# Kernel optimization log

Measured on AMD Instinct MI355X. Metric: run time of the kernel, lower is better.

The kernel has to match this reference:

```python
import jax, jax.numpy as jnp
import numpy as np

N_NODES = 65536
IN_DIM = 256
HIDDEN = 256
NUM_GRAPHS = 128   # B = batch.max()+1; fixed by construction in setup_inputs
MAX_LEN = 1024     # >= max per-graph length (avg 512, binomial tail << 1024)


def _uniform(key, shape, scale):
    return jax.random.uniform(key, shape, jnp.float32, -scale, scale)


def setup_inputs() -> dict:
    key = jax.random.key(0)
    ks = jax.random.split(key, 12)
    x = jax.random.normal(ks[0], (N_NODES, IN_DIM), jnp.float32)
    batch = jnp.sort(jax.random.randint(ks[1], (N_NODES,), 0, NUM_GRAPHS)).astype(jnp.int64)
    s = 1.0 / np.sqrt(HIDDEN)  # torch nn.GRU init: U(-1/sqrt(H), 1/sqrt(H))
    # gate order follows torch: (r, z, n) stacked along first axis -> 3H rows
    params = {
        'W_ih0': _uniform(ks[2], (3 * HIDDEN, IN_DIM), s),
        'W_hh0': _uniform(ks[3], (3 * HIDDEN, HIDDEN), s),
        'b_ih0': _uniform(ks[4], (3 * HIDDEN,), s),
        'b_hh0': _uniform(ks[5], (3 * HIDDEN,), s),
        'W_ih1': _uniform(ks[6], (3 * HIDDEN, HIDDEN), s),
        'W_hh1': _uniform(ks[7], (3 * HIDDEN, HIDDEN), s),
        'b_ih1': _uniform(ks[8], (3 * HIDDEN,), s),
        'b_hh1': _uniform(ks[9], (3 * HIDDEN,), s),
    }
    return {'x': x, 'batch': batch, **params}


def _gru_layer(xs, W_ih, W_hh, b_ih, b_hh):
    # xs: [B, L, D] -> [B, L, H]; torch GRU cell math, gate order (r, z, n)
    B = xs.shape[0]
    H = W_hh.shape[1]
    gx = jnp.einsum('bld,gd->blg', xs, W_ih) + b_ih  # precompute input gates, one big GEMM

    def step(h, gx_t):
        gh = h @ W_hh.T + b_hh
        xr, xz, xn = jnp.split(gx_t, 3, axis=-1)
        hr, hz, hn = jnp.split(gh, 3, axis=-1)
        r = jax.nn.sigmoid(xr + hr)
        z = jax.nn.sigmoid(xz + hz)
        n = jnp.tanh(xn + r * hn)
        h_new = (1.0 - z) * n + z * h
        return h_new, h_new

    h0 = jnp.zeros((B, H), xs.dtype)
    _, hs = jax.lax.scan(step, h0, jnp.swapaxes(gx, 0, 1))  # [L, B, H]
    return jnp.swapaxes(hs, 0, 1)


def reference(x, batch, W_ih0, W_hh0, b_ih0, b_hh0, W_ih1, W_hh1, b_ih1, b_hh1):
    # Ragged per-graph sequences -> padded [B, MAX_LEN, D]. Padding is at the
    # end of each row; GRU is causal so valid positions match the per-graph
    # loop in the original module exactly, and the masked mean ignores padding.
    N, D = x.shape
    b32 = batch.astype(jnp.int32)
    counts = jax.ops.segment_sum(jnp.ones((N,), jnp.float32), b32, num_segments=NUM_GRAPHS)
    starts = jnp.cumsum(counts) - counts              # exclusive prefix sum
    pos = jnp.arange(N, dtype=jnp.float32) - starts[b32]
    pos = pos.astype(jnp.int32)                       # position within graph

    xp = jnp.zeros((NUM_GRAPHS, MAX_LEN, D), x.dtype).at[b32, pos].set(x)
    mask = jnp.zeros((NUM_GRAPHS, MAX_LEN), x.dtype).at[b32, pos].set(1.0)

    h = _gru_layer(xp, W_ih0, W_hh0, b_ih0, b_hh0)
    h = _gru_layer(h, W_ih1, W_hh1, b_ih1, b_hh1)

    denom = jnp.maximum(counts, 1.0)[:, None]
    out = jnp.sum(h * mask[:, :, None], axis=1) / denom  # mean over valid steps
    return out  # dropout is identity at eval
```

## Files before the change

### kernel.cpp

```cpp
#include <hip/hip_runtime.h>
#include <hip/hip_bf16.h>

typedef _Float16 half2_t __attribute__((ext_vector_type(2)));
typedef _Float16 f16x8   __attribute__((ext_vector_type(8)));
typedef float    f32x4   __attribute__((ext_vector_type(4)));
typedef unsigned short u16;
typedef unsigned int   u32;

#define N_NODES 65536
#define IN_DIM  256
#define HIDDEN  256
#define G3      768
#define NGRAPH  128

__device__ __forceinline__ float sigf(float x)    { return 1.f / (1.f + __expf(-x)); }
__device__ __forceinline__ float tanhfast(float x){ return 2.f / (1.f + __expf(-2.f * x)) - 1.f; }

__device__ __forceinline__ void mfma_a(f32x4& acc, const f16x8& a, const f16x8& b) {
    asm("v_mfma_f32_16x16x32_f16 %0, %1, %2, %0" : "+v"(acc) : "a"(a), "v"(b));
}
__device__ __forceinline__ void mfma_v(f32x4& acc, const f16x8& a, const f16x8& b) {
    asm("v_mfma_f32_16x16x32_f16 %0, %1, %2, %0" : "+v"(acc) : "v"(a), "v"(b));
}

__global__ void k_starts(const int* __restrict__ batch, int* __restrict__ starts, int n, int ngraph) {
    int g = blockIdx.x * blockDim.x + threadIdx.x;
    if (g > ngraph) return;
    int stride = (batch[n - 1] == 0) ? 2 : 1;
    if (g == ngraph) { starts[g] = n; return; }
    int lo = 0, hi = n;
    while (lo < hi) { int mid = (lo + hi) >> 1; if (batch[(size_t)mid * stride] < g) lo = mid + 1; else hi = mid; }
    starts[g] = lo;
}

__global__ void k_cvt8(const float* __restrict__ s, u16* __restrict__ d, int n) {
    int t = blockIdx.x * 256 + threadIdx.x;
    int i = t * 8;
    if (i >= n) return;
    float4 a = ((const float4*)(s + i))[0];
    float4 b = ((const float4*)(s + i))[1];
    f16x8 o;
    o[0] = (_Float16)a.x; o[1] = (_Float16)a.y; o[2] = (_Float16)a.z; o[3] = (_Float16)a.w;
    o[4] = (_Float16)b.x; o[5] = (_Float16)b.y; o[6] = (_Float16)b.z; o[7] = (_Float16)b.w;
    *(f16x8*)(d + i) = o;
}

__global__ void k_bias(const float* __restrict__ bih, const float* __restrict__ bhh, float* __restrict__ o) {
    int i = blockIdx.x * 256 + threadIdx.x;
    if (i < G3) o[i] = bih[i] + (i < 512 ? bhh[i] : 0.f);
}

__global__ void k_swz(const float* __restrict__ W, uint4* __restrict__ out) {
    int t = blockIdx.x * 256 + threadIdx.x;
    if (t >= 24576) return;
    int l = t & 63, c = t >> 6;
    int kt = c & 7, t6 = (c >> 3) % 12, wv = c / 96;
    int row = wv * 192 + t6 * 16 + (l & 15);
    int col = kt * 32 + (l >> 4) * 8;
    const float* s = W + row * 256 + col;
    f16x8 o;
#pragma unroll
    for (int q = 0; q < 8; q++) o[q] = (_Float16)s[q];
    out[t] = __builtin_bit_cast(uint4, o);
}

template <typename AT>
__global__ __launch_bounds__(256) void k_gemm(
    const AT* __restrict__ A, const u16* __restrict__ Bm,
    const float* __restrict__ bias, u16* __restrict__ C,
    int M, int N, int K)
{
    __shared__ u16 As[128 * 40];
    __shared__ u16 Bs[128 * 40];
    const int m0 = blockIdx.y * 128, n0 = blockIdx.x * 128;
    const int t = threadIdx.x;
    const int wave = t >> 6, lane = t & 63;
    const int wm = wave & 1, wn = wave >> 1;
    const int lr = lane & 15, lq = lane >> 4;
    f32x4 acc[4][4] = {};
    const int sr = t >> 1, sp = t & 1;
    const AT*  gA = A  + (size_t)(m0 + sr) * K + sp * 16;
    const u16* gB = Bm + (size_t)(n0 + sr) * K + sp * 16;
    u16* sA = As + sr * 40 + sp * 16;
    u16* sB = Bs + sr * 40 + sp * 16;
    for (int kt = 0; kt < K; kt += 32) {
        uint4 av0, av1;
        if constexpr (sizeof(AT) == 4) {
            float4 a0 = ((const float4*)gA)[0], a1 = ((const float4*)gA)[1];
            float4 a2 = ((const float4*)gA)[2], a3 = ((const float4*)gA)[3];
            f16x8 lo, hi;
            lo[0]=(_Float16)a0.x; lo[1]=(_Float16)a0.y; lo[2]=(_Float16)a0.z; lo[3]=(_Float16)a0.w;
            lo[4]=(_Float16)a1.x; lo[5]=(_Float16)a1.y; lo[6]=(_Float16)a1.z; lo[7]=(_Float16)a1.w;
            hi[0]=(_Float16)a2.x; hi[1]=(_Float16)a2.y; hi[2]=(_Float16)a2.z; hi[3]=(_Float16)a2.w;
            hi[4]=(_Float16)a3.x; hi[5]=(_Float16)a3.y; hi[6]=(_Float16)a3.z; hi[7]=(_Float16)a3.w;
            av0 = __builtin_bit_cast(uint4, lo);
            av1 = __builtin_bit_cast(uint4, hi);
        } else {
            av0 = ((const uint4*)gA)[0];
            av1 = ((const uint4*)gA)[1];
        }
        uint4 b0 = ((const uint4*)gB)[0], b1 = ((const uint4*)gB)[1];
        gA += 32; gB += 32;
        __syncthreads();
        ((uint4*)sA)[0] = av0; ((uint4*)sA)[1] = av1;
        ((uint4*)sB)[0] = b0;  ((uint4*)sB)[1] = b1;
        __syncthreads();
        f16x8 af[4], bf[4];
#pragma unroll
        for (int i = 0; i < 4; i++)
            af[i] = *(const f16x8*)(As + (wm * 64 + i * 16 + lr) * 40 + lq * 8);
#pragma unroll
        for (int j = 0; j < 4; j++)
            bf[j] = *(const f16x8*)(Bs + (wn * 64 + j * 16 + lr) * 40 + lq * 8);
#pragma unroll
        for (int i = 0; i < 4; i++)
#pragma unroll
            for (int j = 0; j < 4; j++)
                acc[i][j] = __builtin_amdgcn_mfma_f32_16x16x32_f16(af[i], bf[j], acc[i][j], 0, 0, 0);
    }
#pragma unroll
    for (int i = 0; i < 4; i++) {
        int row = m0 + wm * 64 + i * 16 + lq * 4;
#pragma unroll
        for (int j = 0; j < 4; j++) {
            int col = n0 + wn * 64 + j * 16 + lr;
            float bv = bias[col];
#pragma unroll
            for (int rr = 0; rr < 4; rr++) {
                _Float16 v = (_Float16)(acc[i][j][rr] + bv);
                C[(size_t)(row + rr) * N + col] = __builtin_bit_cast(u16, v);
            }
        }
    }
}

__global__ __attribute__((amdgpu_flat_work_group_size(256, 256), amdgpu_waves_per_eu(1, 1)))
void k_rec(
    const u16* __restrict__ gx,
    const uint4* __restrict__ wsw,
    const float* __restrict__ bhh,
    const int*   __restrict__ starts,
    u16* __restrict__ hout,
    float* __restrict__ out)
{
    __shared__ float gates[G3];
    __shared__ uint4 hpk4[HIDDEN / 8];
    const int g = blockIdx.x;
    const int tid = threadIdx.x;
    const int l = tid & 63, wv = tid >> 6;
    const int start = starts[g];
    const int len = starts[g + 1] - start;
    if (tid < HIDDEN / 8) hpk4[tid] = make_uint4(0, 0, 0, 0);
    f16x8 wa[60], wb[36];
    {
        const uint4* p = wsw + (size_t)wv * 96 * 64 + l;
#pragma unroll
        for (int f = 0; f < 60; f++) {
            f16x8 v = __builtin_bit_cast(f16x8, p[f * 64]);
            asm volatile("" : "+a"(v));
            wa[f] = v;
        }
#pragma unroll
        for (int f = 0; f < 36; f++) {
            f16x8 v = __builtin_bit_cast(f16x8, p[(60 + f) * 64]);
            asm volatile("" : "+v"(v));
            wb[f] = v;
        }
    }
    const _Float16* gxr = (const _Float16*)gx + (size_t)start * G3 + tid;
    u16* hb = hout ? (hout + (size_t)start * HIDDEN + tid) : (u16*)nullptr;
    float hp = 0.f, hs = 0.f;
    const float bn = bhh[512 + tid];
    float gr = 0.f, gz = 0.f, gn = 0.f;
    if (len > 0) { gr = (float)gxr[0]; gz = (float)gxr[256]; gn = (float)gxr[512]; }
    f32x4 acc[12];
#pragma unroll
    for (int t6 = 0; t6 < 12; t6++) acc[t6] = (f32x4){0.f, 0.f, 0.f, 0.f};
    __syncthreads();
    for (int t = 0; t < len; ++t) {
        int tn = t + 1 < len ? t + 1 : len - 1;
        const _Float16* pp = gxr + (u32)tn * G3;
        float pr = (float)pp[0], pz = (float)pp[256], pn = (float)pp[512];
#pragma unroll
        for (int kt = 0; kt < 8; kt++) {
            f16x8 b = __builtin_bit_cast(f16x8, hpk4[kt * 4 + (l >> 4)]);
#pragma unroll
            for (int t6 = 0; t6 < 12; t6++) {
                const int f = t6 * 8 + kt;
                if (f < 60) mfma_a(acc[t6], wa[f], b);
                else        mfma_v(acc[t6], wb[f - 60], b);
            }
        }
        asm volatile("s_nop 7\n\ts_nop 7"
                     : "+v"(acc[0]), "+v"(acc[1]), "+v"(acc[2]), "+v"(acc[3]),
                       "+v"(acc[4]), "+v"(acc[5]), "+v"(acc[6]), "+v"(acc[7]),
                       "+v"(acc[8]), "+v"(acc[9]), "+v"(acc[10]), "+v"(acc[11]));
        if ((l & 15) == 0) {
            int ro = wv * 192 + (l >> 4) * 4;
#pragma unroll
            for (int t6 = 0; t6 < 12; t6++)
                *(f32x4*)&gates[ro + t6 * 16] = acc[t6];
        }
#pragma unroll
        for (int t6 = 0; t6 < 12; t6++) acc[t6] = (f32x4){0.f, 0.f, 0.f, 0.f};
        __syncthreads();
        {
            float r = sigf(gr + gates[tid]);
            float z = sigf(gz + gates[256 + tid]);
            float n = tanhfast(gn + r * (gates[512 + tid] + bn));
            float hnew = (1.f - z) * n + z * hp;
            hp = hnew; hs += hnew;
            _Float16 ph = (_Float16)hnew;
            u16 pk = __builtin_bit_cast(u16, ph);
            ((u16*)hpk4)[tid] = pk;
            if (hb) hb[(u32)t * HIDDEN] = pk;
            gr = pr; gz = pz; gn = pn;
        }
        __syncthreads();
    }
    if (out) {
        float inv = 1.f / (float)(len > 0 ? len : 1);
        out[g * HIDDEN + tid] = hs * inv;
    }
}

extern "C" void kernel_launch(void* const* d_in, const int* in_sizes, int n_in,
                              void* d_out, int out_size, void* d_ws, size_t ws_size,
                              hipStream_t stream)
{
    const float* x     = (const float*)d_in[0];
    const int*   batch = (const int*)d_in[1];
    const float* Wih0  = (const float*)d_in[2];
    const float* Whh0  = (const float*)d_in[3];
    const float* bih0  = (const float*)d_in[4];
    const float* bhh0  = (const float*)d_in[5];
    const float* Wih1  = (const float*)d_in[6];
    const float* Whh1  = (const float*)d_in[7];
    const float* bih1  = (const float*)d_in[8];
    const float* bhh1  = (const float*)d_in[9];
    float* out = (float*)d_out;

    char* ws = (char*)d_ws;
    size_t o = 0;
    int*   starts = (int*)  (ws + o); o += 4096;
    float* bias0  = (float*)(ws + o); o += 4096;
    float* bias1  = (float*)(ws + o); o += 4096;
    u16*   wi0    = (u16*)  (ws + o); o += (size_t)G3 * IN_DIM * 2;
    u16*   wi1    = (u16*)  (ws + o); o += (size_t)G3 * HIDDEN * 2;
    uint4* wsw0   = (uint4*)(ws + o); o += (size_t)G3 * HIDDEN * 2;
    uint4* wsw1   = (uint4*)(ws + o); o += (size_t)G3 * HIDDEN * 2;
    u16*   h0     = (u16*)  (ws + o); o += (size_t)N_NODES * HIDDEN * 2;
    u16*   gxbuf  = (u16*)  (ws + o); o += (size_t)N_NODES * G3 * 2;

    k_starts<<<1, 256, 0, stream>>>(batch, starts, N_NODES, NGRAPH);
    k_bias<<<3, 256, 0, stream>>>(bih0, bhh0, bias0);
    k_bias<<<3, 256, 0, stream>>>(bih1, bhh1, bias1);
    k_cvt8<<<96, 256, 0, stream>>>(Wih0, wi0, G3 * IN_DIM);
    k_cvt8<<<96, 256, 0, stream>>>(Wih1, wi1, G3 * HIDDEN);
    k_swz<<<96, 256, 0, stream>>>(Whh0, wsw0);
    k_swz<<<96, 256, 0, stream>>>(Whh1, wsw1);

    k_gemm<float><<<dim3(G3 / 128, N_NODES / 128), 256, 0, stream>>>(x, wi0, bias0, gxbuf, N_NODES, G3, IN_DIM);
    k_rec<<<NGRAPH, 256, 0, stream>>>(gxbuf, wsw0, bhh0, starts, h0, (float*)nullptr);
    k_gemm<_Float16><<<dim3(G3 / 128, N_NODES / 128), 256, 0, stream>>>((const _Float16*)h0, wi1, bias1, gxbuf, N_NODES, G3, HIDDEN);
    k_rec<<<NGRAPH, 256, 0, stream>>>(gxbuf, wsw1, bhh1, starts, (u16*)nullptr, out);
}
```

Before: 1.856 ms.

## Remap gate rows per wave and double-buffer h to drop a barrier per step

The weight swizzle and gate-store layout are remapped so each wave computes the r/z/n gate rows for exactly the 64 hidden units its own threads consume. That makes the gate exchange through LDS intra-wave, so the barrier between the matmul and the elementwise update can go. The hidden-state buffer is double-buffered, leaving a single lightweight barrier (lgkmcnt wait plus s_barrier) per timestep. Accumulator zeroing is folded into the first MFMA's C operand, and the gx prefetch distance grows to two steps, at the cost of extra registers and reliance on in-order LDS ops within a wave.

After: 1.782 ms. 1.04x faster.

```diff
diff --git a/kernel.cpp b/kernel.cpp
--- a/kernel.cpp
+++ b/kernel.cpp
@@ -21,6 +21,17 @@
 }
 __device__ __forceinline__ void mfma_v(f32x4& acc, const f16x8& a, const f16x8& b) {
     asm("v_mfma_f32_16x16x32_f16 %0, %1, %2, %0" : "+v"(acc) : "v"(a), "v"(b));
+}
+__device__ __forceinline__ void mfma_az(f32x4& acc, const f16x8& a, const f16x8& b, const f32x4& z) {
+    asm("v_mfma_f32_16x16x32_f16 %0, %1, %2, %3" : "=&v"(acc) : "a"(a), "v"(b), "v"(z));
+}
+__device__ __forceinline__ void mfma_vz(f32x4& acc, const f16x8& a, const f16x8& b, const f32x4& z) {
+    asm("v_mfma_f32_16x16x32_f16 %0, %1, %2, %3" : "=&v"(acc) : "v"(a), "v"(b), "v"(z));
+}
+
+__device__ __forceinline__ void wg_barrier_lds() {
+    asm volatile("s_waitcnt lgkmcnt(0)" ::: "memory");
+    __builtin_amdgcn_s_barrier();
 }
 
 __global__ void k_starts(const int* __restrict__ batch, int* __restrict__ starts, int n, int ngraph) {
@@ -55,7 +66,8 @@
     if (t >= 24576) return;
     int l = t & 63, c = t >> 6;
     int kt = c & 7, t6 = (c >> 3) % 12, wv = c / 96;
-    int row = wv * 192 + t6 * 16 + (l & 15);
+    int rg = t6 >> 2, sub = t6 & 3;
+    int row = rg * 256 + wv * 64 + sub * 16 + (l & 15);
     int col = kt * 32 + (l >> 4) * 8;
     const float* s = W + row * 256 + col;
     f16x8 o;
@@ -144,13 +156,13 @@
     float* __restrict__ out)
 {
     __shared__ float gates[G3];
-    __shared__ uint4 hpk4[HIDDEN / 8];
+    __shared__ uint4 hbuf[2][HIDDEN / 8];
     const int g = blockIdx.x;
     const int tid = threadIdx.x;
     const int l = tid & 63, wv = tid >> 6;
     const int start = starts[g];
     const int len = starts[g + 1] - start;
-    if (tid < HIDDEN / 8) hpk4[tid] = make_uint4(0, 0, 0, 0);
+    if (tid < HIDDEN / 8) hbuf[0][tid] = make_uint4(0, 0, 0, 0);
     f16x8 wa[60], wb[36];
     {
         const uint4* p = wsw + (size_t)wv * 96 * 64 + l;
@@ -171,24 +183,34 @@
     u16* hb = hout ? (hout + (size_t)start * HIDDEN + tid) : (u16*)nullptr;
     float hp = 0.f, hs = 0.f;
     const float bn = bhh[512 + tid];
-    float gr = 0.f, gz = 0.f, gn = 0.f;
-    if (len > 0) { gr = (float)gxr[0]; gz = (float)gxr[256]; gn = (float)gxr[512]; }
-    f32x4 acc[12];
-#pragma unroll
-    for (int t6 = 0; t6 < 12; t6++) acc[t6] = (f32x4){0.f, 0.f, 0.f, 0.f};
+    const f32x4 zf = {0.f, 0.f, 0.f, 0.f};
+    float c_r = 0.f, c_z = 0.f, c_n = 0.f;
+    float n_r = 0.f, n_z = 0.f, n_n = 0.f;
+    if (len > 0) {
+        c_r = (float)gxr[0]; c_z = (float)gxr[256]; c_n = (float)gxr[512];
+        int t1 = len > 1 ? 1 : 0;
+        const _Float16* p = gxr + (u32)t1 * G3;
+        n_r = (float)p[0]; n_z = (float)p[256]; n_n = (float)p[512];
+    }
     __syncthreads();
     for (int t = 0; t < len; ++t) {
-        int tn = t + 1 < len ? t + 1 : len - 1;
-        const _Float16* pp = gxr + (u32)tn * G3;
-        float pr = (float)pp[0], pz = (float)pp[256], pn = (float)pp[512];
+        int t2 = t + 2 < len ? t + 2 : len - 1;
+        const _Float16* pp = gxr + (u32)t2 * G3;
+        float l_r = (float)pp[0], l_z = (float)pp[256], l_n = (float)pp[512];
+        f32x4 acc[12];
 #pragma unroll
         for (int kt = 0; kt < 8; kt++) {
-            f16x8 b = __builtin_bit_cast(f16x8, hpk4[kt * 4 + (l >> 4)]);
+            f16x8 b = __builtin_bit_cast(f16x8, hbuf[t & 1][kt * 4 + (l >> 4)]);
 #pragma unroll
             for (int t6 = 0; t6 < 12; t6++) {
                 const int f = t6 * 8 + kt;
-                if (f < 60) mfma_a(acc[t6], wa[f], b);
-                else        mfma_v(acc[t6], wb[f - 60], b);
+                if (kt == 0) {
+                    if (f < 60) mfma_az(acc[t6], wa[f], b, zf);
+                    else        mfma_vz(acc[t6], wb[f - 60], b, zf);
+                } else {
+                    if (f < 60) mfma_a(acc[t6], wa[f], b);
+                    else        mfma_v(acc[t6], wb[f - 60], b);
+                }
             }
         }
         asm volatile("s_nop 7\n\ts_nop 7"
@@ -196,27 +218,26 @@
                        "+v"(acc[4]), "+v"(acc[5]), "+v"(acc[6]), "+v"(acc[7]),
                        "+v"(acc[8]), "+v"(acc[9]), "+v"(acc[10]), "+v"(acc[11]));
         if ((l & 15) == 0) {
-            int ro = wv * 192 + (l >> 4) * 4;
-#pragma unroll
-            for (int t6 = 0; t6 < 12; t6++)
-                *(f32x4*)&gates[ro + t6 * 16] = acc[t6];
-        }
-#pragma unroll
-        for (int t6 = 0; t6 < 12; t6++) acc[t6] = (f32x4){0.f, 0.f, 0.f, 0.f};
-        __syncthreads();
+#pragma unroll
+            for (int t6 = 0; t6 < 12; t6++) {
+                int ro = (t6 >> 2) * 256 + wv * 64 + (t6 & 3) * 16 + (l >> 4) * 4;
+                *(f32x4*)&gates[ro] = acc[t6];
+            }
+        }
         {
-            float r = sigf(gr + gates[tid]);
-            float z = sigf(gz + gates[256 + tid]);
-            float n = tanhfast(gn + r * (gates[512 + tid] + bn));
+            float r = sigf(c_r + gates[tid]);
+            float z = sigf(c_z + gates[256 + tid]);
+            float n = tanhfast(c_n + r * (gates[512 + tid] + bn));
             float hnew = (1.f - z) * n + z * hp;
             hp = hnew; hs += hnew;
             _Float16 ph = (_Float16)hnew;
             u16 pk = __builtin_bit_cast(u16, ph);
-            ((u16*)hpk4)[tid] = pk;
+            ((u16*)hbuf[(t + 1) & 1])[tid] = pk;
             if (hb) hb[(u32)t * HIDDEN] = pk;
-            gr = pr; gz = pz; gn = pn;
-        }
-        __syncthreads();
+            c_r = n_r; c_z = n_z; c_n = n_n;
+            n_r = l_r; n_z = l_z; n_n = l_n;
+        }
+        wg_barrier_lds();
     }
     if (out) {
         float inv = 1.f / (float)(len > 0 ? len : 1);
```
